# Kernel tuning notes

Measured on AMD Instinct MI355X. Metric: run time of the kernel, lower is better.

## Reference

```python
import jax, jax.numpy as jnp
import numpy as np

NEG_SLOPE = 0.01  # nn.LeakyReLU default

def leaky_relu(x):
    return jnp.where(x >= 0, x, NEG_SLOPE * x)

B, C, H, W = 256, 256, 5, 5
L = H * W          # 25 locations (h==5 so no adaptive pooling)
D = C + 1          # +1 coordinate feature
HID = 64
OUT_UNITS = 32

def setup_inputs() -> dict:
    key = jax.random.key(0)
    ks = jax.random.split(key, 9)
    def xavier(k, shape):
        fan_out, fan_in = shape
        a = np.sqrt(6.0 / (fan_in + fan_out))
        return jax.random.uniform(k, shape, jnp.float32, -a, a)
    return {
        "x_img": jax.random.normal(ks[0], (B, C, H, W), jnp.float32),
        "g0_w": xavier(ks[1], (HID, 2 * D)),
        "g0_b": jnp.zeros((HID,), jnp.float32),
        "g1_w": xavier(ks[2], (HID, HID)),
        "g1_b": jnp.zeros((HID,), jnp.float32),
        "post_w": xavier(ks[3], (HID, HID)),
        "post_b": jnp.zeros((HID,), jnp.float32),
        "out_w": xavier(ks[4], (OUT_UNITS, HID)),
        "out_b": jnp.zeros((OUT_UNITS,), jnp.float32),
        "num_step": 0,
    }

def reference(x_img, g0_w, g0_b, g1_w, g1_b, post_w, post_b, out_w, out_b, num_step):
    b, c, h, w = x_img.shape
    length = h * w
    # (b, c, h*w) -> (b, L, c)
    feats = x_img.reshape(b, c, length).transpose(0, 2, 1)
    # append coordinate index feature
    coords = jnp.broadcast_to(jnp.arange(length, dtype=x_img.dtype)[None, :, None], (b, length, 1))
    feats = jnp.concatenate([feats, coords], axis=2)          # (b, L, D)
    d = feats.shape[-1]
    # all-pairs concat: x_i varies over axis 2, x_j over axis 1 (matches torch repeat/cat order)
    x_i = jnp.broadcast_to(feats[:, None, :, :], (b, length, length, d))
    x_j = jnp.broadcast_to(feats[:, :, None, :], (b, length, length, d))
    pair = jnp.concatenate([x_i, x_j], axis=3)                 # (b, L, L, 2D)
    # per-pair MLP g
    out = leaky_relu(jnp.einsum('blmd,kd->blmk', pair, g0_w) + g0_b)
    out = leaky_relu(jnp.einsum('blmk,jk->blmj', out, g1_w) + g1_b)
    # reduce over both pair axes
    out = out.sum(axis=(1, 2))                                 # (b, HID)
    # f
    out = leaky_relu(out @ post_w.T + post_b)
    out = leaky_relu(out @ out_w.T + out_b)                    # (b, OUT_UNITS)
    return out
```

## Files before the change

### kernel.cpp

```cpp
#include <hip/hip_runtime.h>

#define NB 256
#define NC 256
#define NL 25
#define ND 257
#define NHID 64
#define NOUT 32

#define OFF_H0   0
#define OFF_P    24576
#define OFF_B0   30976
#define OFF_SF   31040
#define OFF_Z    31104
#define SMEM_FLOATS 31168

__device__ __forceinline__ float lrelu(float x) {
    return fmaxf(x, 0.0f) + 0.01f * fminf(x, 0.0f);
}

__global__ void k_transpose(const float* __restrict__ g0, float* __restrict__ wt) {
    __shared__ float tile[64][65];
    const int cbase = blockIdx.x * 64;
    const int jh = blockIdx.y;
    const int tid = threadIdx.x;
    for (int i = tid; i < 64 * 64; i += 256) {
        int r = i >> 6;
        int cc = i & 63;
        int c = cbase + cc;
        float v = 0.0f;
        if (c < ND) v = g0[r * (2 * ND) + jh * ND + c];
        tile[r][cc] = v;
    }
    __syncthreads();
    for (int i = tid; i < 64 * 64; i += 256) {
        int cc = i >> 6;
        int r = i & 63;
        int c = cbase + cc;
        if (c < ND) wt[c * 128 + jh * 64 + r] = tile[r][cc];
    }
}

__global__ __launch_bounds__(512, 2)
void k_main(const float* __restrict__ x_img,
            const float* __restrict__ wt,
            const float* __restrict__ g0_b,
            const float* __restrict__ g1_w,
            const float* __restrict__ g1_b,
            const float* __restrict__ post_w,
            const float* __restrict__ post_b,
            const float* __restrict__ out_w,
            const float* __restrict__ out_b,
            float* __restrict__ out)
{
    extern __shared__ float smem[];
    float* h0c = smem + OFF_H0;
    float* xs  = smem + OFF_H0;
    float* red = smem + OFF_H0;
    float* Pb  = smem + OFF_P;
    float* b0s = smem + OFF_B0;
    float* sf  = smem + OFF_SF;
    float* zs  = smem + OFF_Z;

    const int tid  = threadIdx.x;
    const int b    = blockIdx.x;
    const int lane = tid & 63;
    const int wid  = tid >> 6;

    {
        const float4* src = (const float4*)(x_img + (size_t)b * (NC * NL));
        float4* dst = (float4*)xs;
        for (int i = tid; i < 1600; i += 512) dst[i] = src[i];
    }
    if (tid < 64) b0s[tid] = g0_b[tid];
    __syncthreads();

    {
        const int r     = tid & 255;
        const int chalf = tid >> 8;
        const int k4    = r & 15;
        const int uv    = (r >> 4) & 1;
        const int pgrp  = r >> 5;
        const int pstart = pgrp * 3;
        const bool p4   = (pgrp == 7);
        float4 a0 = {0.f,0.f,0.f,0.f}, a1 = a0, a2 = a0, a3 = a0;
        const float4* wp = ((const float4*)wt) + (uv * 16 + k4);
        const float* xrow = xs + pstart;
        const int c0   = chalf ? 128 : 0;
        const int cend = chalf ? 256 : 128;
        #pragma unroll 2
        for (int c = c0; c < cend; ++c) {
            const float4 w4 = wp[c * 32];
            const float f0 = xrow[c * 25 + 0];
            const float f1 = xrow[c * 25 + 1];
            const float f2 = xrow[c * 25 + 2];
            a0.x = fmaf(w4.x, f0, a0.x); a0.y = fmaf(w4.y, f0, a0.y);
            a0.z = fmaf(w4.z, f0, a0.z); a0.w = fmaf(w4.w, f0, a0.w);
            a1.x = fmaf(w4.x, f1, a1.x); a1.y = fmaf(w4.y, f1, a1.y);
            a1.z = fmaf(w4.z, f1, a1.z); a1.w = fmaf(w4.w, f1, a1.w);
            a2.x = fmaf(w4.x, f2, a2.x); a2.y = fmaf(w4.y, f2, a2.y);
            a2.z = fmaf(w4.z, f2, a2.z); a2.w = fmaf(w4.w, f2, a2.w);
            if (p4) {
                const float f3 = xrow[c * 25 + 3];
                a3.x = fmaf(w4.x, f3, a3.x); a3.y = fmaf(w4.y, f3, a3.y);
                a3.z = fmaf(w4.z, f3, a3.z); a3.w = fmaf(w4.w, f3, a3.w);
            }
        }
        if (chalf) {
            const float4 w4 = wp[256 * 32];
            const float f0 = (float)(pstart + 0);
            const float f1 = (float)(pstart + 1);
            const float f2 = (float)(pstart + 2);
            a0.x = fmaf(w4.x, f0, a0.x); a0.y = fmaf(w4.y, f0, a0.y);
            a0.z = fmaf(w4.z, f0, a0.z); a0.w = fmaf(w4.w, f0, a0.w);
            a1.x = fmaf(w4.x, f1, a1.x); a1.y = fmaf(w4.y, f1, a1.y);
            a1.z = fmaf(w4.z, f1, a1.z); a1.w = fmaf(w4.w, f1, a1.w);
            a2.x = fmaf(w4.x, f2, a2.x); a2.y = fmaf(w4.y, f2, a2.y);
            a2.z = fmaf(w4.z, f2, a2.z); a2.w = fmaf(w4.w, f2, a2.w);
            if (p4) {
                const float f3 = (float)(pstart + 3);
                a3.x = fmaf(w4.x, f3, a3.x); a3.y = fmaf(w4.y, f3, a3.y);
                a3.z = fmaf(w4.z, f3, a3.z); a3.w = fmaf(w4.w, f3, a3.w);
            }
        }
        float* dst = Pb + (chalf * 2 + uv) * 1600;
        *(float4*)&dst[(pstart + 0) * 64 + k4 * 4] = a0;
        *(float4*)&dst[(pstart + 1) * 64 + k4 * 4] = a1;
        *(float4*)&dst[(pstart + 2) * 64 + k4 * 4] = a2;
        if (p4) *(float4*)&dst[(pstart + 3) * 64 + k4 * 4] = a3;
    }
    __syncthreads();

    float acc[32];
    #pragma unroll
    for (int j = 0; j < 32; ++j) acc[j] = 0.f;
    const int jbase = __builtin_amdgcn_readfirstlane((wid & 1) * 32);

    #pragma unroll 1
    for (int ch = 0; ch < 2; ++ch) {
        const int cbase = ch ? 384 : 0;
        const int slots = ch ? 256 : 384;
        __syncthreads();
        const float4* P4 = (const float4*)Pb;
        const int rounds = (slots * 16) >> 9;
        #pragma unroll 1
        for (int rr = 0; rr < rounds; ++rr) {
            const int idx = rr * 512 + tid;
            const int k4 = idx & 15;
            const int lp = idx >> 4;
            int pp = cbase + lp; pp = (pp > 624) ? 624 : pp;
            const int l = (pp * 5243) >> 17;
            const int m = pp - l * 25;
            const float4 u0 = P4[         m * 16 + k4];
            const float4 v0 = P4[ 400 +   l * 16 + k4];
            const float4 u1 = P4[ 800 +   m * 16 + k4];
            const float4 v1 = P4[1200 +   l * 16 + k4];
            const float4 b4 = *(const float4*)&b0s[k4 * 4];
            float4 h;
            h.x = lrelu(u0.x + u1.x + v0.x + v1.x + b4.x);
            h.y = lrelu(u0.y + u1.y + v0.y + v1.y + b4.y);
            h.z = lrelu(u0.z + u1.z + v0.z + v1.z + b4.z);
            h.w = lrelu(u0.w + u1.w + v0.w + v1.w + b4.w);
            *(float4*)&h0c[lp * 64 + ((k4 ^ (lp & 15)) << 2)] = h;
        }
        __syncthreads();
        #pragma unroll 1
        for (int T = wid; T < 20; T += 8) {
            const int batch = T >> 1;
            if (ch ? (batch < 6) : (batch >= 6)) continue;
            const int pp = batch * 64 + lane;
            const bool ok = pp < 625;
            const int lp = ((pp > 624) ? 624 : pp) - cbase;
            float4 h[16];
            const int hb = lp * 64;
            const int sw = lp & 15;
            #pragma unroll
            for (int k = 0; k < 16; ++k)
                h[k] = *(const float4*)&h0c[hb + ((k ^ sw) << 2)];
            #pragma unroll
            for (int j = 0; j < 32; ++j) {
                const float4* __restrict__ gr =
                    (const float4*)(g1_w + (size_t)(jbase + j) * 64);
                float4 q0 = {0.f,0.f,0.f,0.f}, q1 = q0, q2 = q0, q3 = q0;
                #pragma unroll
                for (int k = 0; k < 4; ++k) {
                    float4 g;
                    g = gr[k*4+0];
                    q0.x = fmaf(g.x, h[k*4+0].x, q0.x); q0.y = fmaf(g.y, h[k*4+0].y, q0.y);
                    q0.z = fmaf(g.z, h[k*4+0].z, q0.z); q0.w = fmaf(g.w, h[k*4+0].w, q0.w);
                    g = gr[k*4+1];
                    q1.x = fmaf(g.x, h[k*4+1].x, q1.x); q1.y = fmaf(g.y, h[k*4+1].y, q1.y);
                    q1.z = fmaf(g.z, h[k*4+1].z, q1.z); q1.w = fmaf(g.w, h[k*4+1].w, q1.w);
                    g = gr[k*4+2];
                    q2.x = fmaf(g.x, h[k*4+2].x, q2.x); q2.y = fmaf(g.y, h[k*4+2].y, q2.y);
                    q2.z = fmaf(g.z, h[k*4+2].z, q2.z); q2.w = fmaf(g.w, h[k*4+2].w, q2.w);
                    g = gr[k*4+3];
                    q3.x = fmaf(g.x, h[k*4+3].x, q3.x); q3.y = fmaf(g.y, h[k*4+3].y, q3.y);
                    q3.z = fmaf(g.z, h[k*4+3].z, q3.z); q3.w = fmaf(g.w, h[k*4+3].w, q3.w);
                }
                const float s0 = (q0.x + q0.y) + (q0.z + q0.w);
                const float s1 = (q1.x + q1.y) + (q1.z + q1.w);
                const float s2 = (q2.x + q2.y) + (q2.z + q2.w);
                const float s3 = (q3.x + q3.y) + (q3.z + q3.w);
                const float d  = (s0 + s1) + (s2 + s3);
                const float t  = lrelu(d + g1_b[jbase + j]);
                acc[j] += ok ? t : 0.0f;
            }
        }
    }

    __syncthreads();
    {
        const int col = ((wid >> 1) << 6) + lane;
        #pragma unroll
        for (int j = 0; j < 32; ++j)
            red[(jbase + j) * 264 + col] = acc[j];
    }
    __syncthreads();
    {
        const int j = tid >> 3, seg = tid & 7;
        const float* rp = red + j * 264 + seg;
        float s = 0.f;
        #pragma unroll
        for (int i = 0; i < 32; ++i) s += rp[i * 8];
        s += __shfl_xor(s, 1, 64);
        s += __shfl_xor(s, 2, 64);
        s += __shfl_xor(s, 4, 64);
        if (seg == 0) sf[j] = s;
    }
    __syncthreads();

    if (tid < 64) {
        float a = post_b[tid];
        #pragma unroll 8
        for (int k = 0; k < 64; ++k) a = fmaf(post_w[tid * 64 + k], sf[k], a);
        zs[tid] = lrelu(a);
        if (tid < 32) {
            float a2 = out_b[tid];
            #pragma unroll 8
            for (int k = 0; k < 64; ++k) a2 = fmaf(out_w[tid * 64 + k], zs[k], a2);
            out[b * NOUT + tid] = lrelu(a2);
        }
    }
}

extern "C" void kernel_launch(void* const* d_in, const int* in_sizes, int n_in,
                              void* d_out, int out_size, void* d_ws, size_t ws_size,
                              hipStream_t stream) {
    const float* x_img  = (const float*)d_in[0];
    const float* g0_w   = (const float*)d_in[1];
    const float* g0_b   = (const float*)d_in[2];
    const float* g1_w   = (const float*)d_in[3];
    const float* g1_b   = (const float*)d_in[4];
    const float* post_w = (const float*)d_in[5];
    const float* post_b = (const float*)d_in[6];
    const float* out_w  = (const float*)d_in[7];
    const float* out_b  = (const float*)d_in[8];
    float* out = (float*)d_out;
    float* wt  = (float*)d_ws;

    hipFuncSetAttribute((const void*)k_main,
                        hipFuncAttributeMaxDynamicSharedMemorySize,
                        SMEM_FLOATS * 4);

    k_transpose<<<dim3(5, 2), 256, 0, stream>>>(g0_w, wt);
    k_main<<<dim3(NB), 512, SMEM_FLOATS * 4, stream>>>(x_img, wt, g0_b, g1_w, g1_b,
                                                       post_w, post_b, out_w, out_b, out);
}
```

Before: 167.4 us.

## Repartition layer-1 MLP so each wave owns 8 output rows over all pairs

Result: slower. 217.6 us (+30.0%).

```diff
diff --git a/kernel.cpp b/kernel.cpp
--- a/kernel.cpp
+++ b/kernel.cpp
@@ -8,11 +8,11 @@
 #define NOUT 32
 
 #define OFF_H0   0
-#define OFF_P    24576
-#define OFF_B0   30976
-#define OFF_SF   31040
-#define OFF_Z    31104
-#define SMEM_FLOATS 31168
+#define OFF_P    20480
+#define OFF_B0   26880
+#define OFF_RED  26944
+#define OFF_Z    27008
+#define SMEM_FLOATS 27072
 
 __device__ __forceinline__ float lrelu(float x) {
     return fmaxf(x, 0.0f) + 0.01f * fminf(x, 0.0f);
@@ -55,10 +55,9 @@
     extern __shared__ float smem[];
     float* h0c = smem + OFF_H0;
     float* xs  = smem + OFF_H0;
-    float* red = smem + OFF_H0;
     float* Pb  = smem + OFF_P;
     float* b0s = smem + OFF_B0;
-    float* sf  = smem + OFF_SF;
+    float* red = smem + OFF_RED;
     float* zs  = smem + OFF_Z;
 
     const int tid  = threadIdx.x;
@@ -130,20 +129,18 @@
     }
     __syncthreads();
 
-    float acc[32];
+    float acc[8];
     #pragma unroll
-    for (int j = 0; j < 32; ++j) acc[j] = 0.f;
-    const int jbase = __builtin_amdgcn_readfirstlane((wid & 1) * 32);
+    for (int jj = 0; jj < 8; ++jj) acc[jj] = 0.f;
+    const int wrow = __builtin_amdgcn_readfirstlane(wid * 8);
+    const int sw = lane & 15;
 
     #pragma unroll 1
     for (int ch = 0; ch < 2; ++ch) {
-        const int cbase = ch ? 384 : 0;
-        const int slots = ch ? 256 : 384;
-        __syncthreads();
+        const int cbase = ch ? 320 : 0;
         const float4* P4 = (const float4*)Pb;
-        const int rounds = (slots * 16) >> 9;
         #pragma unroll 1
-        for (int rr = 0; rr < rounds; ++rr) {
+        for (int rr = 0; rr < 10; ++rr) {
             const int idx = rr * 512 + tid;
             const int k4 = idx & 15;
             const int lp = idx >> 4;
@@ -164,75 +161,56 @@
         }
         __syncthreads();
         #pragma unroll 1
-        for (int T = wid; T < 20; T += 8) {
-            const int batch = T >> 1;
-            if (ch ? (batch < 6) : (batch >= 6)) continue;
-            const int pp = batch * 64 + lane;
+        for (int t = 0; t < 5; ++t) {
+            const int lp = t * 64 + lane;
+            const int pp = cbase + lp;
             const bool ok = pp < 625;
-            const int lp = ((pp > 624) ? 624 : pp) - cbase;
+            const int hb = lp * 64;
             float4 h[16];
-            const int hb = lp * 64;
-            const int sw = lp & 15;
             #pragma unroll
             for (int k = 0; k < 16; ++k)
                 h[k] = *(const float4*)&h0c[hb + ((k ^ sw) << 2)];
             #pragma unroll
-            for (int j = 0; j < 32; ++j) {
-                const float4* __restrict__ gr =
-                    (const float4*)(g1_w + (size_t)(jbase + j) * 64);
-                float4 q0 = {0.f,0.f,0.f,0.f}, q1 = q0, q2 = q0, q3 = q0;
+            for (int jj = 0; jj < 8; ++jj) {
+                const int row = wrow + jj;
+                const float* __restrict__ gr = g1_w + (size_t)row * 64;
+                float d0 = 0.f, d1 = 0.f, d2 = 0.f, d3 = 0.f;
                 #pragma unroll
-                for (int k = 0; k < 4; ++k) {
-                    float4 g;
-                    g = gr[k*4+0];
-                    q0.x = fmaf(g.x, h[k*4+0].x, q0.x); q0.y = fmaf(g.y, h[k*4+0].y, q0.y);
-                    q0.z = fmaf(g.z, h[k*4+0].z, q0.z); q0.w = fmaf(g.w, h[k*4+0].w, q0.w);
-                    g = gr[k*4+1];
-                    q1.x = fmaf(g.x, h[k*4+1].x, q1.x); q1.y = fmaf(g.y, h[k*4+1].y, q1.y);
-                    q1.z = fmaf(g.z, h[k*4+1].z, q1.z); q1.w = fmaf(g.w, h[k*4+1].w, q1.w);
-                    g = gr[k*4+2];
-                    q2.x = fmaf(g.x, h[k*4+2].x, q2.x); q2.y = fmaf(g.y, h[k*4+2].y, q2.y);
-                    q2.z = fmaf(g.z, h[k*4+2].z, q2.z); q2.w = fmaf(g.w, h[k*4+2].w, q2.w);
-                    g = gr[k*4+3];
-                    q3.x = fmaf(g.x, h[k*4+3].x, q3.x); q3.y = fmaf(g.y, h[k*4+3].y, q3.y);
-                    q3.z = fmaf(g.z, h[k*4+3].z, q3.z); q3.w = fmaf(g.w, h[k*4+3].w, q3.w);
+                for (int kq = 0; kq < 16; ++kq) {
+                    d0 = fmaf(gr[kq * 4 + 0], h[kq].x, d0);
+                    d1 = fmaf(gr[kq * 4 + 1], h[kq].y, d1);
+                    d2 = fmaf(gr[kq * 4 + 2], h[kq].z, d2);
+                    d3 = fmaf(gr[kq * 4 + 3], h[kq].w, d3);
                 }
-                const float s0 = (q0.x + q0.y) + (q0.z + q0.w);
-                const float s1 = (q1.x + q1.y) + (q1.z + q1.w);
-                const float s2 = (q2.x + q2.y) + (q2.z + q2.w);
-                const float s3 = (q3.x + q3.y) + (q3.z + q3.w);
-                const float d  = (s0 + s1) + (s2 + s3);
-                const float t  = lrelu(d + g1_b[jbase + j]);
-                acc[j] += ok ? t : 0.0f;
+                const float d = (d0 + d1) + (d2 + d3);
+                const float tv = lrelu(d + g1_b[row]);
+                acc[jj] += ok ? tv : 0.0f;
             }
         }
-    }
-
-    __syncthreads();
+        __syncthreads();
+    }
+
     {
-        const int col = ((wid >> 1) << 6) + lane;
+        float vout = 0.f;
         #pragma unroll
-        for (int j = 0; j < 32; ++j)
-            red[(jbase + j) * 264 + col] = acc[j];
-    }
-    __syncthreads();
-    {
-        const int j = tid >> 3, seg = tid & 7;
-        const float* rp = red + j * 264 + seg;
-        float s = 0.f;
-        #pragma unroll
-        for (int i = 0; i < 32; ++i) s += rp[i * 8];
-        s += __shfl_xor(s, 1, 64);
-        s += __shfl_xor(s, 2, 64);
-        s += __shfl_xor(s, 4, 64);
-        if (seg == 0) sf[j] = s;
+        for (int jj = 0; jj < 8; ++jj) {
+            float s = acc[jj];
+            s += __shfl_xor(s, 1, 64);
+            s += __shfl_xor(s, 2, 64);
+            s += __shfl_xor(s, 4, 64);
+            s += __shfl_xor(s, 8, 64);
+            s += __shfl_xor(s, 16, 64);
+            s += __shfl_xor(s, 32, 64);
+            vout = (lane == jj) ? s : vout;
+        }
+        if (lane < 8) red[wid * 8 + lane] = vout;
     }
     __syncthreads();
 
     if (tid < 64) {
         float a = post_b[tid];
         #pragma unroll 8
-        for (int k = 0; k < 64; ++k) a = fmaf(post_w[tid * 64 + k], sf[k], a);
+        for (int k = 0; k < 64; ++k) a = fmaf(post_w[tid * 64 + k], red[k], a);
         zs[tid] = lrelu(a);
         if (tid < 32) {
             float a2 = out_b[tid];
```
